# Performance work log

Hardware: AMD Instinct MI355X
Metric: run time of the kernel (lower is better)

The kernel has to match this reference:

```python
import jax, jax.numpy as jnp
import numpy as np

N = 50000
E = 800000
D_IN = 128
D_OUT = 128


def setup_inputs() -> dict:
    key = jax.random.key(0)
    k1, k2, k3 = jax.random.split(key, 3)
    seq = jax.random.normal(k1, (N, D_IN), dtype=jnp.float32)
    edge_index = jax.random.randint(k2, (2, E), 0, N, dtype=jnp.int32)
    # Glorot-ish init for the GCNConv linear weight [in, out]
    W = jax.random.normal(k3, (D_IN, D_OUT), dtype=jnp.float32) * (1.0 / np.sqrt(D_IN))
    b = jnp.zeros((D_OUT,), dtype=jnp.float32)
    prelu_w = jnp.full((1,), 0.25, dtype=jnp.float32)
    return {"seq": seq, "edge_index": edge_index, "W": W, "b": b, "prelu_w": prelu_w}


def reference(seq, edge_index, W, b, prelu_w):
    # GCNConv: linear transform, add self-loops, symmetric normalization,
    # scatter-add aggregation, bias; then PReLU activation.
    n = seq.shape[0]
    xW = seq @ W  # [N, D_OUT]

    # add self-loops
    loop = jnp.arange(n, dtype=edge_index.dtype)
    row = jnp.concatenate([edge_index[0], loop])  # source
    col = jnp.concatenate([edge_index[1], loop])  # target

    # degree of target nodes (edge weight = 1)
    deg = jax.ops.segment_sum(jnp.ones_like(col, dtype=xW.dtype), col, num_segments=n)
    dinv = jnp.where(deg > 0, jax.lax.rsqrt(deg), 0.0)
    norm = dinv[row] * dinv[col]  # [E+N]

    msg = xW[row] * norm[:, None]  # gather + scale
    out = jax.ops.segment_sum(msg, col, num_segments=n)  # scatter-add
    out = out + b

    # PReLU with single shared weight
    return jnp.where(out > 0, out, prelu_w[0] * out)
```

## Files before the change

kernel.cpp:

```cpp
#include <hip/hip_runtime.h>

constexpr int D = 128;
constexpr int CAP = 64;
constexpr int OVFCAP = 65536;

__device__ __forceinline__ unsigned short f2bf(float f) {
    unsigned u = __float_as_uint(f);
    u += 0x7fffu + ((u >> 16) & 1u);
    return (unsigned short)(u >> 16);
}

__global__ __launch_bounds__(256) void k_place_gemm(
        const int* __restrict__ row, const int* __restrict__ col,
        int* __restrict__ deg, int* __restrict__ slots,
        int* __restrict__ ovfCnt, int2* __restrict__ ovf, int E,
        int gemmBlocks,
        const float* __restrict__ seq, const float* __restrict__ W,
        unsigned short* __restrict__ y16, int n) {
    __shared__ float sS[32 * D];

    int b = (int)blockIdx.x;
    int half = b >> 1;
    bool isGemm = ((b & 1) == 0) && (half < gemmBlocks);

    if (!isGemm) {
        int pIdx = (b < 2 * gemmBlocks) ? half : (b - gemmBlocks);
        int e = pIdx * 256 + threadIdx.x;
        if (e < E) {
            int c = col[e];
            int r = row[e];
            int p = atomicAdd(&deg[c], 1);
            if (p < CAP) {
                slots[(size_t)c * CAP + p] = r;
            } else {
                int o = atomicAdd(ovfCnt, 1);
                if (o < OVFCAP) ovf[o] = make_int2(r, c);
            }
        }
        return;
    }

    int row0 = half * 32;
    int rows = n - row0; if (rows > 32) rows = 32;

    {
        const float4* src = (const float4*)(seq + (size_t)row0 * D);
        float4* dst = (float4*)sS;
        int nf4 = rows * (D / 4);
        for (int i = threadIdx.x; i < nf4; i += 256) dst[i] = src[i];
    }
    __syncthreads();

    int cg = threadIdx.x & 31;
    int rg = threadIdx.x >> 5;
    const float4* W4 = (const float4*)W;

    float4 acc[4];
    #pragma unroll
    for (int j = 0; j < 4; ++j) acc[j] = make_float4(0.f, 0.f, 0.f, 0.f);

    #pragma unroll 4
    for (int k = 0; k < D; ++k) {
        float4 w = W4[k * 32 + cg];
        #pragma unroll
        for (int j = 0; j < 4; ++j) {
            float s = sS[(rg * 4 + j) * D + k];
            acc[j].x = fmaf(s, w.x, acc[j].x);
            acc[j].y = fmaf(s, w.y, acc[j].y);
            acc[j].z = fmaf(s, w.z, acc[j].z);
            acc[j].w = fmaf(s, w.w, acc[j].w);
        }
    }

    #pragma unroll
    for (int j = 0; j < 4; ++j) {
        int g = row0 + rg * 4 + j;
        if (g < n) {
            ushort4 o;
            o.x = f2bf(acc[j].x);
            o.y = f2bf(acc[j].y);
            o.z = f2bf(acc[j].z);
            o.w = f2bf(acc[j].w);
            *(ushort4*)(y16 + (size_t)g * D + cg * 4) = o;
        }
    }
}

__global__ __launch_bounds__(256) void k_agg(
        const int* __restrict__ slots, const int* __restrict__ deg,
        const int* __restrict__ ovfCnt, const int2* __restrict__ ovf,
        const unsigned short* __restrict__ y16,
        const float* __restrict__ b, const float* __restrict__ pw,
        float* __restrict__ out, int n) {
    int wid = (blockIdx.x * 256 + threadIdx.x) >> 6;
    if (wid >= n) return;
    int lane = threadIdx.x & 63;

    int cntf = deg[wid];
    int cnt = cntf < CAP ? cntf : CAP;
    float dc = rsqrtf((float)(cntf + 1));

    unsigned sv = *(const unsigned*)(y16 + (size_t)wid * D + 2 * lane);
    float ax0 = __uint_as_float(sv << 16) * dc;
    float ay0 = __uint_as_float(sv & 0xffff0000u) * dc;
    float ax1 = 0.f, ay1 = 0.f, ax2 = 0.f, ay2 = 0.f, ax3 = 0.f, ay3 = 0.f;
    float ax4 = 0.f, ay4 = 0.f, ax5 = 0.f, ay5 = 0.f, ax6 = 0.f, ay6 = 0.f;
    float ax7 = 0.f, ay7 = 0.f;

    int my = (lane < cnt) ? slots[(size_t)wid * CAP + lane] : 0;

    int k = 0;
    for (; k + 7 < cnt; k += 8) {
        int r0 = __shfl(my, k);
        int r1 = __shfl(my, k + 1);
        int r2 = __shfl(my, k + 2);
        int r3 = __shfl(my, k + 3);
        int r4 = __shfl(my, k + 4);
        int r5 = __shfl(my, k + 5);
        int r6 = __shfl(my, k + 6);
        int r7 = __shfl(my, k + 7);
        int g0 = deg[r0]; int g1 = deg[r1]; int g2 = deg[r2]; int g3 = deg[r3];
        int g4 = deg[r4]; int g5 = deg[r5]; int g6 = deg[r6]; int g7 = deg[r7];
        unsigned v0 = *(const unsigned*)(y16 + (size_t)r0 * D + 2 * lane);
        unsigned v1 = *(const unsigned*)(y16 + (size_t)r1 * D + 2 * lane);
        unsigned v2 = *(const unsigned*)(y16 + (size_t)r2 * D + 2 * lane);
        unsigned v3 = *(const unsigned*)(y16 + (size_t)r3 * D + 2 * lane);
        unsigned v4 = *(const unsigned*)(y16 + (size_t)r4 * D + 2 * lane);
        unsigned v5 = *(const unsigned*)(y16 + (size_t)r5 * D + 2 * lane);
        unsigned v6 = *(const unsigned*)(y16 + (size_t)r6 * D + 2 * lane);
        unsigned v7 = *(const unsigned*)(y16 + (size_t)r7 * D + 2 * lane);
        float dr0 = rsqrtf((float)(g0 + 1));
        float dr1 = rsqrtf((float)(g1 + 1));
        float dr2 = rsqrtf((float)(g2 + 1));
        float dr3 = rsqrtf((float)(g3 + 1));
        float dr4 = rsqrtf((float)(g4 + 1));
        float dr5 = rsqrtf((float)(g5 + 1));
        float dr6 = rsqrtf((float)(g6 + 1));
        float dr7 = rsqrtf((float)(g7 + 1));
        ax0 = fmaf(__uint_as_float(v0 << 16), dr0, ax0); ay0 = fmaf(__uint_as_float(v0 & 0xffff0000u), dr0, ay0);
        ax1 = fmaf(__uint_as_float(v1 << 16), dr1, ax1); ay1 = fmaf(__uint_as_float(v1 & 0xffff0000u), dr1, ay1);
        ax2 = fmaf(__uint_as_float(v2 << 16), dr2, ax2); ay2 = fmaf(__uint_as_float(v2 & 0xffff0000u), dr2, ay2);
        ax3 = fmaf(__uint_as_float(v3 << 16), dr3, ax3); ay3 = fmaf(__uint_as_float(v3 & 0xffff0000u), dr3, ay3);
        ax4 = fmaf(__uint_as_float(v4 << 16), dr4, ax4); ay4 = fmaf(__uint_as_float(v4 & 0xffff0000u), dr4, ay4);
        ax5 = fmaf(__uint_as_float(v5 << 16), dr5, ax5); ay5 = fmaf(__uint_as_float(v5 & 0xffff0000u), dr5, ay5);
        ax6 = fmaf(__uint_as_float(v6 << 16), dr6, ax6); ay6 = fmaf(__uint_as_float(v6 & 0xffff0000u), dr6, ay6);
        ax7 = fmaf(__uint_as_float(v7 << 16), dr7, ax7); ay7 = fmaf(__uint_as_float(v7 & 0xffff0000u), dr7, ay7);
    }
    for (; k < cnt; ++k) {
        int r = __shfl(my, k);
        float dr = rsqrtf((float)(deg[r] + 1));
        unsigned v = *(const unsigned*)(y16 + (size_t)r * D + 2 * lane);
        ax0 = fmaf(__uint_as_float(v << 16), dr, ax0);
        ay0 = fmaf(__uint_as_float(v & 0xffff0000u), dr, ay0);
    }

    if (cntf > CAP) {
        int m = *ovfCnt; if (m > OVFCAP) m = OVFCAP;
        for (int j = 0; j < m; ++j) {
            int2 pr = ovf[j];
            if (pr.y == wid) {
                float dr = rsqrtf((float)(deg[pr.x] + 1));
                unsigned v = *(const unsigned*)(y16 + (size_t)pr.x * D + 2 * lane);
                ax0 = fmaf(__uint_as_float(v << 16), dr, ax0);
                ay0 = fmaf(__uint_as_float(v & 0xffff0000u), dr, ay0);
            }
        }
    }

    float sx = ((ax0 + ax1) + (ax2 + ax3)) + ((ax4 + ax5) + (ax6 + ax7));
    float sy = ((ay0 + ay1) + (ay2 + ay3)) + ((ay4 + ay5) + (ay6 + ay7));

    float2 bb = *(const float2*)(b + 2 * lane);
    float p = pw[0];
    float vx = sx * dc + bb.x;
    float vy = sy * dc + bb.y;
    vx = vx > 0.f ? vx : p * vx;
    vy = vy > 0.f ? vy : p * vy;
    *(float2*)(out + (size_t)wid * D + 2 * lane) = make_float2(vx, vy);
}

extern "C" void kernel_launch(void* const* d_in, const int* in_sizes, int n_in,
                              void* d_out, int out_size, void* d_ws, size_t ws_size,
                              hipStream_t stream) {
    const float* seq = (const float*)d_in[0];
    const int*   ei  = (const int*)d_in[1];
    const float* W   = (const float*)d_in[2];
    const float* b   = (const float*)d_in[3];
    const float* pw  = (const float*)d_in[4];
    int n = in_sizes[0] / D;
    int E = in_sizes[1] / 2;

    float* out = (float*)d_out;

    auto align = [](size_t x) { return (x + 255) & ~(size_t)255; };
    char* p = (char*)d_ws;
    unsigned short* y16 = (unsigned short*)p; p += align((size_t)n * D * sizeof(unsigned short));
    int*  deg    = (int*)p;   size_t degBytes = align((size_t)n * sizeof(int)); p += degBytes;
    int*  ovfCnt = (int*)p;   p += 256;
    int2* ovf    = (int2*)p;  p += align((size_t)OVFCAP * sizeof(int2));
    int*  slots  = (int*)p;   p += align((size_t)n * CAP * sizeof(int));

    hipMemsetAsync(deg, 0, degBytes + 256, stream);

    int GB = (n + 31) / 32;
    int PB = (E + 255) / 256;
    k_place_gemm<<<GB + PB, 256, 0, stream>>>(
        ei, ei + E, deg, slots, ovfCnt, ovf, E, GB, seq, W, y16, n);

    k_agg<<<(unsigned)(((long long)n * 64 + 255) / 256), 256, 0, stream>>>(
        slots, deg, ovfCnt, ovf, y16, b, pw, out, n);
}
```

Baseline: 109.6 us.

## Enlarge GEMM tile to 64 rows with shared-memory W staging; place two edges per thread

```diff
diff --git a/kernel.cpp b/kernel.cpp
--- a/kernel.cpp
+++ b/kernel.cpp
@@ -17,7 +17,8 @@
         int gemmBlocks,
         const float* __restrict__ seq, const float* __restrict__ W,
         unsigned short* __restrict__ y16, int n) {
-    __shared__ float sS[32 * D];
+    __shared__ float sS[64 * D];
+    __shared__ float sW[16 * D];
 
     int b = (int)blockIdx.x;
     int half = b >> 1;
@@ -25,23 +26,29 @@
 
     if (!isGemm) {
         int pIdx = (b < 2 * gemmBlocks) ? half : (b - gemmBlocks);
-        int e = pIdx * 256 + threadIdx.x;
-        if (e < E) {
+        int t = pIdx * 256 + threadIdx.x;
+        int e = 2 * t;
+        if (e + 1 < E) {
+            int2 c2 = *(const int2*)(col + e);
+            int2 r2 = *(const int2*)(row + e);
+            int p0 = atomicAdd(&deg[c2.x], 1);
+            int p1 = atomicAdd(&deg[c2.y], 1);
+            if (p0 < CAP) slots[(size_t)c2.x * CAP + p0] = r2.x;
+            else { int o = atomicAdd(ovfCnt, 1); if (o < OVFCAP) ovf[o] = make_int2(r2.x, c2.x); }
+            if (p1 < CAP) slots[(size_t)c2.y * CAP + p1] = r2.y;
+            else { int o = atomicAdd(ovfCnt, 1); if (o < OVFCAP) ovf[o] = make_int2(r2.y, c2.y); }
+        } else if (e < E) {
             int c = col[e];
             int r = row[e];
             int p = atomicAdd(&deg[c], 1);
-            if (p < CAP) {
-                slots[(size_t)c * CAP + p] = r;
-            } else {
-                int o = atomicAdd(ovfCnt, 1);
-                if (o < OVFCAP) ovf[o] = make_int2(r, c);
-            }
+            if (p < CAP) slots[(size_t)c * CAP + p] = r;
+            else { int o = atomicAdd(ovfCnt, 1); if (o < OVFCAP) ovf[o] = make_int2(r, c); }
         }
         return;
     }
 
-    int row0 = half * 32;
-    int rows = n - row0; if (rows > 32) rows = 32;
+    int row0 = half * 64;
+    int rows = n - row0; if (rows > 64) rows = 64;
 
     {
         const float4* src = (const float4*)(seq + (size_t)row0 * D);
@@ -49,32 +56,41 @@
         int nf4 = rows * (D / 4);
         for (int i = threadIdx.x; i < nf4; i += 256) dst[i] = src[i];
     }
-    __syncthreads();
 
     int cg = threadIdx.x & 31;
     int rg = threadIdx.x >> 5;
-    const float4* W4 = (const float4*)W;
-
-    float4 acc[4];
+    float4 acc[8];
     #pragma unroll
-    for (int j = 0; j < 4; ++j) acc[j] = make_float4(0.f, 0.f, 0.f, 0.f);
-
-    #pragma unroll 4
-    for (int k = 0; k < D; ++k) {
-        float4 w = W4[k * 32 + cg];
+    for (int j = 0; j < 8; ++j) acc[j] = make_float4(0.f, 0.f, 0.f, 0.f);
+
+    for (int kc = 0; kc < 8; ++kc) {
+        __syncthreads();
+        {
+            const float4* wsrc = (const float4*)(W + (size_t)kc * 16 * D);
+            float4* wdst = (float4*)sW;
+            wdst[threadIdx.x]       = wsrc[threadIdx.x];
+            wdst[threadIdx.x + 256] = wsrc[threadIdx.x + 256];
+        }
+        __syncthreads();
+        int kbase = kc * 16;
         #pragma unroll
-        for (int j = 0; j < 4; ++j) {
-            float s = sS[(rg * 4 + j) * D + k];
-            acc[j].x = fmaf(s, w.x, acc[j].x);
-            acc[j].y = fmaf(s, w.y, acc[j].y);
-            acc[j].z = fmaf(s, w.z, acc[j].z);
-            acc[j].w = fmaf(s, w.w, acc[j].w);
+        for (int k2 = 0; k2 < 16; ++k2) {
+            float4 w = ((const float4*)sW)[k2 * 32 + cg];
+            int k = kbase + k2;
+            #pragma unroll
+            for (int j = 0; j < 8; ++j) {
+                float s = sS[(rg * 8 + j) * D + k];
+                acc[j].x = fmaf(s, w.x, acc[j].x);
+                acc[j].y = fmaf(s, w.y, acc[j].y);
+                acc[j].z = fmaf(s, w.z, acc[j].z);
+                acc[j].w = fmaf(s, w.w, acc[j].w);
+            }
         }
     }
 
     #pragma unroll
-    for (int j = 0; j < 4; ++j) {
-        int g = row0 + rg * 4 + j;
+    for (int j = 0; j < 8; ++j) {
+        int g = row0 + rg * 8 + j;
         if (g < n) {
             ushort4 o;
             o.x = f2bf(acc[j].x);
@@ -202,8 +218,8 @@
 
     hipMemsetAsync(deg, 0, degBytes + 256, stream);
 
-    int GB = (n + 31) / 32;
-    int PB = (E + 255) / 256;
+    int GB = (n + 63) / 64;
+    int PB = (E + 511) / 512;
     k_place_gemm<<<GB + PB, 256, 0, stream>>>(
         ei, ei + E, deg, slots, ovfCnt, ovf, E, GB, seq, W, y16, n);
 
```

Result: faster. 100.3 us (-8.5%).
